# Optimization experiments

Measured on AMD Instinct MI355X. Metric: run time of the kernel, lower is better.

## Reference

```python
import jax, jax.numpy as jnp
import numpy as np

NUM_HEADS = 16
DIM = 1024
HEAD_DIM = DIM // NUM_HEADS
SCALE = HEAD_DIM ** -0.5


def setup_inputs() -> dict:
    key = jax.random.key(0)
    ks = jax.random.split(key, 6)
    b, n = 2, 1024
    x = jax.random.normal(ks[0], (b, n, DIM), dtype=jnp.float32)
    Wq = jax.random.normal(ks[1], (DIM, DIM), dtype=jnp.float32) * 0.02
    bq = jnp.zeros((DIM,), dtype=jnp.float32)
    Wkv = jax.random.normal(ks[2], (2 * DIM, DIM), dtype=jnp.float32) * 0.02
    bkv = jnp.zeros((2 * DIM,), dtype=jnp.float32)
    Wp = jax.random.normal(ks[3], (DIM, DIM), dtype=jnp.float32) * 0.02
    bp = jnp.zeros((DIM,), dtype=jnp.float32)
    return {"x": x, "Wq": Wq, "bq": bq, "Wkv": Wkv, "bkv": bkv, "Wp": Wp, "bp": bp}


def reference(x, Wq, bq, Wkv, bkv, Wp, bp):
    b, n, c = x.shape
    h, dh = NUM_HEADS, HEAD_DIM
    # self-attention: y = x
    q = (x @ Wq.T + bq).reshape(b, n, h, dh)              # bnhd
    kv = (x @ Wkv.T + bkv).reshape(b, n, 2, h, dh)
    k, v = kv[:, :, 0], kv[:, :, 1]                       # bmhd each
    attn = jnp.einsum('bnhd,bmhd->bnmh', q, k) * SCALE    # bnmh scores
    attn = jax.nn.softmax(attn, axis=2)                   # softmax over m
    out = jnp.einsum('bnmh,bmhd->bnhd', attn, v).reshape(b, n, c)
    out = out @ Wp.T + bp
    return (out, attn)
```

## Files before the change

kernel.cpp:

```cpp
#include <hip/hip_runtime.h>
#include <hip/hip_bf16.h>
#include <stdint.h>


#define NB   2
#define SEQ  1024
#define CDIM 1024
#define NH   16
#define HD   64
#define ROWS (NB*SEQ)
#define ATT_SCALE 0.125f

typedef __attribute__((ext_vector_type(8))) short bf16x8;
typedef __attribute__((ext_vector_type(4))) float f32x4;

#define MFMA16(a,b,c) __builtin_amdgcn_mfma_f32_16x16x32_bf16((a),(b),(c),0,0,0)

static __device__ __forceinline__ unsigned short f2bf(float f) {
  uint32_t x = __builtin_bit_cast(uint32_t, f);
  return (unsigned short)((x + 0x7fffu + ((x >> 16) & 1u)) >> 16);
}
static __device__ __forceinline__ float bf2f(unsigned short u) {
  uint32_t x = ((uint32_t)u) << 16;
  return __builtin_bit_cast(float, x);
}

static __device__ __forceinline__ void gl_lds16(const unsigned short* g,
                                                unsigned short* l) {
  __builtin_amdgcn_global_load_lds(
      (const __attribute__((address_space(1))) unsigned int*)g,
      (__attribute__((address_space(3))) unsigned int*)l,
      16, 0, 0);
}

__global__ __launch_bounds__(256) void k_convert(
    const float* __restrict__ x, const float* __restrict__ Wq,
    const float* __restrict__ Wkv, const float* __restrict__ Wp,
    unsigned short* __restrict__ Xhi, unsigned short* __restrict__ Xlo,
    unsigned short* __restrict__ Whi, unsigned short* __restrict__ Wlo)
{
  const int NX4 = ROWS*CDIM/4;
  const int NW4 = 4096*CDIM/4;
  int i = blockIdx.x*256 + threadIdx.x;
  float4 f;
  unsigned short* dh;
  unsigned short* dl;
  size_t o4;
  if (i < NX4) {
    f = ((const float4*)x)[i];
    dh = Xhi; dl = Xlo; o4 = (size_t)i*4;
  } else if (i < NX4 + NW4) {
    int w4 = i - NX4;
    int j = w4 >> 8;
    int c4 = w4 & 255;
    const float* ws = (j < 1024) ? Wq + (size_t)j*1024
                    : (j < 3072) ? Wkv + (size_t)(j-1024)*1024
                                 : Wp + (size_t)(j-3072)*1024;
    f = ((const float4*)ws)[c4];
    dh = Whi; dl = Wlo; o4 = (size_t)w4*4;
  } else return;
  float fv[4] = {f.x, f.y, f.z, f.w};
  unsigned int hp[2], lp[2];
  #pragma unroll
  for (int e = 0; e < 2; e++) {
    unsigned short h0 = f2bf(fv[e*2]),   l0 = f2bf(fv[e*2]   - bf2f(h0));
    unsigned short h1 = f2bf(fv[e*2+1]), l1 = f2bf(fv[e*2+1] - bf2f(h1));
    hp[e] = (unsigned)h0 | ((unsigned)h1 << 16);
    lp[e] = (unsigned)l0 | ((unsigned)l1 << 16);
  }
  *(uint2*)(dh + o4) = make_uint2(hp[0], hp[1]);
  *(uint2*)(dl + o4) = make_uint2(lp[0], lp[1]);
}

__global__ __launch_bounds__(256) void k_gemm_qkv(
    const unsigned short* __restrict__ Xhi, const unsigned short* __restrict__ Xlo,
    const unsigned short* __restrict__ Whi, const unsigned short* __restrict__ Wlo,
    const float* __restrict__ bq, const float* __restrict__ bkv,
    unsigned short* __restrict__ Qhi, unsigned short* __restrict__ Qlo,
    unsigned short* __restrict__ Khi, unsigned short* __restrict__ Klo,
    unsigned short* __restrict__ Vthi, unsigned short* __restrict__ Vtlo)
{
  __shared__ unsigned short smem[12288];
  unsigned short* sAh = smem;
  unsigned short* sAl = smem + 4096;
  unsigned short* sBh = smem + 8192;
  unsigned short* sBl = smem + 10240;
  const int tid = threadIdx.x, lane = tid & 63, wave = tid >> 6;
  const int wm = wave & 1, wn = wave >> 1;
  const int bn = blockIdx.x * 64, bm = blockIdx.y * 128;
  const int r = lane & 15, q = lane >> 4;
  const int crow = lane >> 2;
  const int cgsw = ((lane & 3) ^ ((crow >> 1) & 3)) * 8;
  const int qsw = (q ^ ((r >> 1) & 3)) * 8;

  f32x4 acc[4][2];
  #pragma unroll
  for (int i = 0; i < 4; i++)
    #pragma unroll
    for (int j = 0; j < 2; j++) {
      acc[i][j][0]=0.f; acc[i][j][1]=0.f; acc[i][j][2]=0.f; acc[i][j][3]=0.f;
    }

  for (int k0 = 0; k0 < CDIM; k0 += 32) {
    #pragma unroll
    for (int t = 0; t < 6; t++) {
      int c = wave + t*4;
      const unsigned short* gb; unsigned short* sb; int rr, grow;
      if (c < 8)        { gb=Xhi; sb=sAh; rr=c;    grow=bm; }
      else if (c < 16)  { gb=Xlo; sb=sAl; rr=c-8;  grow=bm; }
      else if (c < 20)  { gb=Whi; sb=sBh; rr=c-16; grow=bn; }
      else              { gb=Wlo; sb=sBl; rr=c-20; grow=bn; }
      int row = rr*16 + crow;
      gl_lds16(gb + (size_t)(grow + row)*CDIM + k0 + cgsw, sb + rr*512);
    }
    __syncthreads();
    bf16x8 ah[4], al[4], bh[2], bl[2];
    #pragma unroll
    for (int i = 0; i < 4; i++) {
      int oa = (wm*64 + i*16 + r)*32 + qsw;
      ah[i] = *(const bf16x8*)(sAh + oa);
      al[i] = *(const bf16x8*)(sAl + oa);
    }
    #pragma unroll
    for (int j = 0; j < 2; j++) {
      int ob = (wn*32 + j*16 + r)*32 + qsw;
      bh[j] = *(const bf16x8*)(sBh + ob);
      bl[j] = *(const bf16x8*)(sBl + ob);
    }
    #pragma unroll
    for (int i = 0; i < 4; i++)
      #pragma unroll
      for (int j = 0; j < 2; j++) {
        acc[i][j] = MFMA16(ah[i], bh[j], acc[i][j]);
        acc[i][j] = MFMA16(ah[i], bl[j], acc[i][j]);
        acc[i][j] = MFMA16(al[i], bh[j], acc[i][j]);
      }
    __syncthreads();
  }

  const int seg = bn >> 10;
  const float* bias = (seg == 0) ? (bq + bn) : (bkv + (bn - 1024));
  const float scl = (seg == 0) ? ATT_SCALE : 1.0f;
  float bj[2] = { bias[wn*32 + r], bias[wn*32 + 16 + r] };

  if (seg < 2) {
    unsigned short* dh = (seg == 0) ? Qhi : Khi;
    unsigned short* dl = (seg == 0) ? Qlo : Klo;
    const int ncol = bn & 1023;
    #pragma unroll
    for (int p = 0; p < 2; p++) {
      #pragma unroll
      for (int i = 0; i < 4; i++)
        #pragma unroll
        for (int j = 0; j < 2; j++)
          #pragma unroll
          for (int t = 0; t < 4; t++) {
            int m_l = wm*64 + i*16 + q*4 + t;
            int n_l = wn*32 + j*16 + r;
            float v2 = (acc[i][j][t] + bj[j]) * scl;
            unsigned short hv = f2bf(v2);
            unsigned short val = (p == 0) ? hv : f2bf(v2 - bf2f(hv));
            smem[m_l*72 + n_l] = val;
          }
      __syncthreads();
      unsigned short* dst = (p == 0) ? dh : dl;
      #pragma unroll
      for (int u = 0; u < 4; u++) {
        int s = u*256 + tid;
        int m_l = s >> 3, nseg = s & 7;
        uint4 vv = *(const uint4*)(smem + m_l*72 + nseg*8);
        *(uint4*)(dst + (size_t)(bm + m_l)*1024 + ncol + nseg*8) = vv;
      }
      __syncthreads();
    }
  } else {
    const int h = (bn - 2048) >> 6;
    const int b = bm >> 10, mm = bm & 1023;
    const size_t vtb = ((size_t)((b*NH + h)*HD))*SEQ + mm;
    #pragma unroll
    for (int p = 0; p < 2; p++) {
      #pragma unroll
      for (int i = 0; i < 4; i++)
        #pragma unroll
        for (int j = 0; j < 2; j++)
          #pragma unroll
          for (int t = 0; t < 4; t++) {
            int m_l = wm*64 + i*16 + q*4 + t;
            int d_l = wn*32 + j*16 + r;
            float v2 = acc[i][j][t] + bj[j];
            unsigned short hv = f2bf(v2);
            unsigned short val = (p == 0) ? hv : f2bf(v2 - bf2f(hv));
            smem[d_l*136 + m_l] = val;
          }
      __syncthreads();
      unsigned short* dst = (p == 0) ? Vthi : Vtlo;
      #pragma unroll
      for (int u = 0; u < 4; u++) {
        int s = u*256 + tid;
        int d_l = s >> 4, mseg = s & 15;
        uint4 vv = *(const uint4*)(smem + d_l*136 + mseg*8);
        *(uint4*)(dst + vtb + (size_t)d_l*SEQ + mseg*8) = vv;
      }
      __syncthreads();
    }
  }
}

struct EpiOut {
  const float* bp; float* out;
  __device__ __forceinline__ void operator()(int m, int n, float v) const {
    out[(size_t)m*1024 + n] = v + bp[n];
  }
};

template <int BM, int BN, int WM, int WN, class Epi>
__device__ __forceinline__ void gemm_core(
    const unsigned short* __restrict__ Ahi, const unsigned short* __restrict__ Alo, int lda,
    const unsigned short* __restrict__ Bhi, const unsigned short* __restrict__ Blo, int ldb,
    int K, const Epi& epi)
{
  constexpr int WAVES = WM*WN;
  constexpr int FM = BM/(WM*16), FN = BN/(WN*16);
  constexpr int CA = BM/16, CB = BN/16;
  constexpr int TOT = 2*(CA+CB);
  __shared__ unsigned short sAh[BM*32], sAl[BM*32], sBh[BN*32], sBl[BN*32];
  const int tid  = threadIdx.x;
  const int lane = tid & 63, wave = tid >> 6;
  const int wm = wave % WM, wn = wave / WM;
  const int bn = blockIdx.x * BN, bm = blockIdx.y * BM;
  const int r = lane & 15, q = lane >> 4;
  const int crow = lane >> 2;
  const int cgsw = ((lane & 3) ^ ((crow >> 1) & 3)) * 8;
  const int qsw = (q ^ ((r >> 1) & 3)) * 8;

  f32x4 acc[FM][FN];
  #pragma unroll
  for (int i = 0; i < FM; i++)
    #pragma unroll
    for (int j = 0; j < FN; j++) {
      acc[i][j][0]=0.f; acc[i][j][1]=0.f; acc[i][j][2]=0.f; acc[i][j][3]=0.f;
    }

  for (int k0 = 0; k0 < K; k0 += 32) {
    #pragma unroll
    for (int t = 0; t < TOT/WAVES; t++) {
      int c = wave + t*WAVES;
      const unsigned short* gb; unsigned short* sb; int rr, grow, ld;
      if (c < CA)            { gb=Ahi; sb=sAh; rr=c;         grow=bm; ld=lda; }
      else if (c < 2*CA)     { gb=Alo; sb=sAl; rr=c-CA;      grow=bm; ld=lda; }
      else if (c < 2*CA+CB)  { gb=Bhi; sb=sBh; rr=c-2*CA;    grow=bn; ld=ldb; }
      else                   { gb=Blo; sb=sBl; rr=c-2*CA-CB; grow=bn; ld=ldb; }
      int row = rr*16 + crow;
      gl_lds16(gb + (size_t)(grow + row)*ld + k0 + cgsw, sb + rr*512);
    }
    __syncthreads();
    bf16x8 ah[FM], al[FM], bh[FN], bl[FN];
    #pragma unroll
    for (int i = 0; i < FM; i++) {
      int oa = (wm*(BM/WM) + i*16 + r)*32 + qsw;
      ah[i] = *(const bf16x8*)(sAh + oa);
      al[i] = *(const bf16x8*)(sAl + oa);
    }
    #pragma unroll
    for (int j = 0; j < FN; j++) {
      int ob = (wn*(BN/WN) + j*16 + r)*32 + qsw;
      bh[j] = *(const bf16x8*)(sBh + ob);
      bl[j] = *(const bf16x8*)(sBl + ob);
    }
    #pragma unroll
    for (int i = 0; i < FM; i++)
      #pragma unroll
      for (int j = 0; j < FN; j++) {
        acc[i][j] = MFMA16(ah[i], bh[j], acc[i][j]);
        acc[i][j] = MFMA16(ah[i], bl[j], acc[i][j]);
        acc[i][j] = MFMA16(al[i], bh[j], acc[i][j]);
      }
    __syncthreads();
  }
  #pragma unroll
  for (int i = 0; i < FM; i++)
    #pragma unroll
    for (int j = 0; j < FN; j++)
      #pragma unroll
      for (int t = 0; t < 4; t++)
        epi(bm + wm*(BM/WM) + i*16 + q*4 + t, bn + wn*(BN/WN) + j*16 + r, acc[i][j][t]);
}

__global__ __launch_bounds__(512) void k_gemm_out(
    const unsigned short* OAhi, const unsigned short* OAlo,
    const unsigned short* Wphi, const unsigned short* Wplo,
    const float* bp, float* out)
{
  EpiOut e{bp, out};
  gemm_core<128,64,4,2>(OAhi, OAlo, CDIM, Wphi, Wplo, CDIM, CDIM, e);
}

__global__ __launch_bounds__(512, 4) void k_logits_softmax(
    const unsigned short* __restrict__ Qhi, const unsigned short* __restrict__ Qlo,
    const unsigned short* __restrict__ Khi, const unsigned short* __restrict__ Klo,
    unsigned short* __restrict__ P, float* __restrict__ F)
{
  int id = blockIdx.x + 32*(blockIdx.y + 16*blockIdx.z);
  id = (id & 7)*128 + (id >> 3);
  const int nt = id & 31, h = (id >> 5) & 15, b = id >> 9;
  const int n0 = nt*32;
  const int col0 = h*HD;
  __shared__ unsigned short sQ[2*32*64];
  __shared__ unsigned short sK[2][2*8192];
  __shared__ float redm[2][8][32];
  __shared__ float reds[8][32];
  __shared__ float musd[32][8];
  const int tid = threadIdx.x, lane = tid & 63, wave = tid >> 6;
  const int r = lane & 15, q = lane >> 4;
  const int drow = lane >> 3, dseg = (lane & 7) ^ drow;
  const int sw = r & 7;
  const size_t qrow0 = (size_t)b*SEQ + n0;
  const size_t krow0 = (size_t)b*SEQ;

  auto stageK = [&](int c, int buf) {
    unsigned short* dst = sK[buf];
    #pragma unroll
    for (int u = 0; u < 4; u++) {
      int cc = wave*4 + u;
      int p = cc >> 4, t = cc & 15;
      const unsigned short* g = p ? Klo : Khi;
      gl_lds16(g + (krow0 + (size_t)c*128 + t*8 + drow)*CDIM + col0 + dseg*8,
               dst + p*8192 + t*512);
    }
  };

  {
    int p = wave >> 2, t = wave & 3;
    const unsigned short* g = p ? Qlo : Qhi;
    gl_lds16(g + (qrow0 + t*8 + drow)*CDIM + col0 + dseg*8,
             sQ + p*2048 + t*512);
    stageK(0, 0);
  }
  __syncthreads();

  bf16x8 qh[2][2], ql[2][2];
  #pragma unroll
  for (int nf = 0; nf < 2; nf++)
    #pragma unroll
    for (int ks = 0; ks < 2; ks++) {
      int phys = (nf*16 + r)*64 + (((ks*4 + q) ^ sw))*8;
      qh[nf][ks] = *(const bf16x8*)(sQ + phys);
      ql[nf][ks] = *(const bf16x8*)(sQ + 2048 + phys);
    }

  const int mb = wave*16;
  float m_run[2] = {-1e30f, -1e30f}, s_run[2] = {0.f, 0.f};
  const size_t pbase = ((size_t)(b*NH + h)*SEQ + n0)*SEQ;

  for (int c = 0; c < 8; c++) {
    if (c < 7) stageK(c+1, (c+1)&1);
    const unsigned short* cur = sK[c&1];
    bf16x8 kh[2], kl[2];
    #pragma unroll
    for (int ks = 0; ks < 2; ks++) {
      int phys = (mb + r)*64 + (((ks*4 + q) ^ sw))*8;
      kh[ks] = *(const bf16x8*)(cur + phys);
      kl[ks] = *(const bf16x8*)(cur + 8192 + phys);
    }
    f32x4 acc[2];
    #pragma unroll
    for (int nf = 0; nf < 2; nf++) {
      acc[nf][0]=0.f; acc[nf][1]=0.f; acc[nf][2]=0.f; acc[nf][3]=0.f;
      #pragma unroll
      for (int ks = 0; ks < 2; ks++) {
        acc[nf] = MFMA16(kh[ks], qh[nf][ks], acc[nf]);
        acc[nf] = MFMA16(kl[ks], qh[nf][ks], acc[nf]);
        acc[nf] = MFMA16(kh[ks], ql[nf][ks], acc[nf]);
      }
    }
    float wmax[2];
    #pragma unroll
    for (int nf = 0; nf < 2; nf++) {
      float v = fmaxf(fmaxf(acc[nf][0], acc[nf][1]), fmaxf(acc[nf][2], acc[nf][3]));
      v = fmaxf(v, __shfl_xor(v, 16));
      v = fmaxf(v, __shfl_xor(v, 32));
      wmax[nf] = v;
    }
    if (q == 0) { redm[c&1][wave][r] = wmax[0]; redm[c&1][wave][16+r] = wmax[1]; }
    __syncthreads();
    #pragma unroll
    for (int nf = 0; nf < 2; nf++) {
      int row = nf*16 + r;
      float mc = redm[c&1][0][row];
      #pragma unroll
      for (int w2 = 1; w2 < 8; w2++) mc = fmaxf(mc, redm[c&1][w2][row]);
      float mnew = fmaxf(m_run[nf], mc);
      unsigned s0 = (unsigned)(__expf(acc[nf][0]-mnew)*65535.f + 0.5f);
      unsigned s1 = (unsigned)(__expf(acc[nf][1]-mnew)*65535.f + 0.5f);
      unsigned s2 = (unsigned)(__expf(acc[nf][2]-mnew)*65535.f + 0.5f);
      unsigned s3 = (unsigned)(__expf(acc[nf][3]-mnew)*65535.f + 0.5f);
      *(uint2*)(P + pbase + (size_t)row*SEQ + c*128 + mb + q*4) =
          make_uint2(s0 | (s1 << 16), s2 | (s3 << 16));
      s_run[nf] = s_run[nf]*__expf(m_run[nf]-mnew) + (float)(s0+s1+s2+s3);
      m_run[nf] = mnew;
      if (wave == 0 && q == 0) musd[row][c] = mnew;
    }
  }

  #pragma unroll
  for (int nf = 0; nf < 2; nf++) {
    float s = s_run[nf];
    s += __shfl_xor(s, 16);
    s += __shfl_xor(s, 32);
    if (q == 0) reds[wave][nf*16 + r] = s;
  }
  __syncthreads();
  if (tid < 32) {
    int row = tid;
    float S = 0.f;
    #pragma unroll
    for (int w2 = 0; w2 < 8; w2++) S += reds[w2][row];
    float mfin = musd[row][7];
    float inv = 1.0f / S;
    size_t fb = ((size_t)(b*NH + h)*SEQ + n0 + row)*8;
    #pragma unroll
    for (int c = 0; c < 8; c++)
      F[fb + c] = __expf(musd[row][c] - mfin) * inv;
  }
}

__global__ __launch_bounds__(256) void k_attn_write(
    const unsigned short* __restrict__ P, const float* __restrict__ F,
    float* __restrict__ attn)
{
  int T = blockIdx.x*256 + threadIdx.x;
  int b = T >> 20, rem = T & 1048575;
  int n = rem >> 10, m = rem & 1023;
  int c = m >> 7;
  const size_t pb = ((size_t)(b*NH)*SEQ + n)*SEQ + m;
  const size_t fb = ((size_t)(b*NH)*SEQ + n)*8 + c;
  float v[16];
  #pragma unroll
  for (int h = 0; h < 16; h++)
    v[h] = (float)P[pb + (size_t)h*SEQ*SEQ] * F[fb + (size_t)h*SEQ*8];
  size_t ob = ((size_t)(b*SEQ + n)*SEQ + m)*16;
  #pragma unroll
  for (int g = 0; g < 4; g++)
    *(float4*)(attn + ob + g*4) = make_float4(v[g*4], v[g*4+1], v[g*4+2], v[g*4+3]);
}

__global__ __launch_bounds__(256) void k_pv(
    const unsigned short* __restrict__ P, const float* __restrict__ F,
    const unsigned short* __restrict__ Vthi, const unsigned short* __restrict__ Vtlo,
    unsigned short* __restrict__ OAhi, unsigned short* __restrict__ OAlo)
{
  int id = blockIdx.x + 16*(blockIdx.y + 16*blockIdx.z);
  id = (id & 7)*64 + (id >> 3);
  int nt = id & 15, h = (id >> 4) & 15, b = id >> 8;
  int n0 = nt * 64;
  __shared__ unsigned short sPa[64*32], sPb[64*32], sVh[64*32], sVl[64*32];
  const int tid = threadIdx.x, lane = tid & 63, wave = tid >> 6;
  const int wm = wave & 1, wn = wave >> 1;
  const int r = lane & 15, q = lane >> 4;
  const int crow = lane >> 2;
  const int cgsw = ((lane & 3) ^ ((crow >> 1) & 3)) * 8;
  const int qsw = (q ^ ((r >> 1) & 3)) * 8;
  const size_t pbase = ((size_t)(b*NH + h))*SEQ*SEQ;
  const size_t vbase = ((size_t)(b*NH + h))*HD*SEQ;
  const size_t fbase = ((size_t)(b*NH + h))*SEQ*8;

  f32x4 acc[2][2], accF[2][2];
  #pragma unroll
  for (int i = 0; i < 2; i++)
    #pragma unroll
    for (int j = 0; j < 2; j++) {
      acc[i][j][0]=0.f; acc[i][j][1]=0.f; acc[i][j][2]=0.f; acc[i][j][3]=0.f;
      accF[i][j][0]=0.f; accF[i][j][1]=0.f; accF[i][j][2]=0.f; accF[i][j][3]=0.f;
    }

  for (int k0 = 0; k0 < SEQ; k0 += 32) {
    #pragma unroll
    for (int t = 0; t < 2; t++) {
      int c = wave + t*4;
      const unsigned short* gb = (c < 4) ? Vthi : Vtlo;
      unsigned short* sb = (c < 4) ? (unsigned short*)sVh : (unsigned short*)sVl;
      int rr = c & 3;
      int row = rr*16 + crow;
      gl_lds16(gb + vbase + (size_t)row*SEQ + k0 + cgsw, sb + rr*512);
    }
    {
      int row = tid >> 2, g = tid & 3, ch = g * 8;
      int gp = (g ^ ((row >> 1) & 3)) * 8;
      uint4 v = *(const uint4*)(P + pbase + (size_t)(n0 + row)*SEQ + k0 + ch);
      unsigned int wds[4] = {v.x, v.y, v.z, v.w};
      unsigned int pa[4], pb4[4];
      #pragma unroll
      for (int e = 0; e < 4; e++) {
        unsigned int lo16 = wds[e] & 0xFFFFu;
        unsigned int hi16 = wds[e] >> 16;
        unsigned int a0 = __builtin_bit_cast(uint32_t, (float)(lo16 & 0xFF00u)) >> 16;
        unsigned int b0 = __builtin_bit_cast(uint32_t, (float)(lo16 & 0x00FFu)) >> 16;
        unsigned int a1 = __builtin_bit_cast(uint32_t, (float)(hi16 & 0xFF00u)) >> 16;
        unsigned int b1 = __builtin_bit_cast(uint32_t, (float)(hi16 & 0x00FFu)) >> 16;
        pa[e]  = a0 | (a1 << 16);
        pb4[e] = b0 | (b1 << 16);
      }
      *(uint4*)(sPa + row*32 + gp) = make_uint4(pa[0],pa[1],pa[2],pa[3]);
      *(uint4*)(sPb + row*32 + gp) = make_uint4(pb4[0],pb4[1],pb4[2],pb4[3]);
    }
    __syncthreads();
    bf16x8 pa[2], pb2[2], vh[2], vl[2];
    #pragma unroll
    for (int i = 0; i < 2; i++) {
      int off = (wm*32 + i*16 + r)*32 + qsw;
      pa[i]  = *(const bf16x8*)(sPa + off);
      pb2[i] = *(const bf16x8*)(sPb + off);
    }
    #pragma unroll
    for (int j = 0; j < 2; j++) {
      int off = (wn*32 + j*16 + r)*32 + qsw;
      vh[j] = *(const bf16x8*)(sVh + off);
      vl[j] = *(const bf16x8*)(sVl + off);
    }
    #pragma unroll
    for (int i = 0; i < 2; i++)
      #pragma unroll
      for (int j = 0; j < 2; j++) {
        acc[i][j] = MFMA16(pa[i],  vh[j], acc[i][j]);
        acc[i][j] = MFMA16(pb2[i], vh[j], acc[i][j]);
        acc[i][j] = MFMA16(pa[i],  vl[j], acc[i][j]);
      }
    if ((k0 & 127) == 96) {
      int c = k0 >> 7;
      #pragma unroll
      for (int i = 0; i < 2; i++)
        #pragma unroll
        for (int t = 0; t < 4; t++) {
          int nn = n0 + wm*32 + i*16 + q*4 + t;
          float Fv = F[fbase + (size_t)nn*8 + c];
          #pragma unroll
          for (int j = 0; j < 2; j++) {
            accF[i][j][t] += acc[i][j][t] * Fv;
            acc[i][j][t] = 0.f;
          }
        }
    }
    __syncthreads();
  }
  #pragma unroll
  for (int i = 0; i < 2; i++)
    #pragma unroll
    for (int t = 0; t < 4; t++) {
      int nn = n0 + wm*32 + i*16 + q*4 + t;
      #pragma unroll
      for (int j = 0; j < 2; j++) {
        int d = wn*32 + j*16 + r;
        float val = accF[i][j][t];
        size_t o = (size_t)(b*SEQ + nn)*CDIM + h*HD + d;
        unsigned short hb = f2bf(val);
        OAhi[o] = hb; OAlo[o] = f2bf(val - bf2f(hb));
      }
    }
}

extern "C" void kernel_launch(void* const* d_in, const int* in_sizes, int n_in,
                              void* d_out, int out_size, void* d_ws, size_t ws_size,
                              hipStream_t stream)
{
  const float* x   = (const float*)d_in[0];
  const float* Wq  = (const float*)d_in[1];
  const float* bq  = (const float*)d_in[2];
  const float* Wkv = (const float*)d_in[3];
  const float* bkv = (const float*)d_in[4];
  const float* Wp  = (const float*)d_in[5];
  const float* bp  = (const float*)d_in[6];

  float* out  = (float*)d_out;
  float* attn = out + (size_t)ROWS*CDIM;

  char* w = (char*)d_ws;
  unsigned short* Xhi  = (unsigned short*)w; w += (size_t)ROWS*CDIM*2;
  unsigned short* Xlo  = (unsigned short*)w; w += (size_t)ROWS*CDIM*2;
  unsigned short* Whi  = (unsigned short*)w; w += (size_t)4096*CDIM*2;
  unsigned short* Wlo  = (unsigned short*)w; w += (size_t)4096*CDIM*2;
  unsigned short* Qhi  = (unsigned short*)w; w += (size_t)ROWS*CDIM*2;
  unsigned short* Qlo  = (unsigned short*)w; w += (size_t)ROWS*CDIM*2;
  unsigned short* Khi  = (unsigned short*)w; w += (size_t)ROWS*CDIM*2;
  unsigned short* Klo  = (unsigned short*)w; w += (size_t)ROWS*CDIM*2;
  unsigned short* Vthi = (unsigned short*)w; w += (size_t)NB*NH*HD*SEQ*2;
  unsigned short* Vtlo = (unsigned short*)w; w += (size_t)NB*NH*HD*SEQ*2;
  unsigned short* OAhi = (unsigned short*)w; w += (size_t)ROWS*CDIM*2;
  unsigned short* OAlo = (unsigned short*)w; w += (size_t)ROWS*CDIM*2;
  unsigned short* P    = (unsigned short*)w; w += (size_t)NB*NH*SEQ*SEQ*2;
  float*          Ftab = (float*)w;          w += (size_t)NB*NH*SEQ*8*4;

  k_convert<<<dim3((ROWS*CDIM/4 + 4096*CDIM/4)/256), 256, 0, stream>>>(
      x, Wq, Wkv, Wp, Xhi, Xlo, Whi, Wlo);

  k_gemm_qkv<<<dim3(3072/64, 2048/128), 256, 0, stream>>>(
      Xhi, Xlo, Whi, Wlo, bq, bkv, Qhi, Qlo, Khi, Klo, Vthi, Vtlo);

  k_logits_softmax<<<dim3(SEQ/32, NH, NB), 512, 0, stream>>>(
      Qhi, Qlo, Khi, Klo, P, Ftab);

  k_pv<<<dim3(SEQ/64, NH, NB), 256, 0, stream>>>(P, Ftab, Vthi, Vtlo, OAhi, OAlo);

  k_gemm_out<<<dim3(1024/64, 2048/128), 512, 0, stream>>>(
      OAhi, OAlo, Whi + (size_t)3072*CDIM, Wlo + (size_t)3072*CDIM, bp, out);

  k_attn_write<<<dim3((NB*SEQ*SEQ)/256), 256, 0, stream>>>(P, Ftab, attn);
}
```

Baseline: 350.2 us.

## Fuse logits/softmax and PV into one flash-style attention kernel

Merges the logits+softmax kernel with the separate P·V kernel into one kernel that keeps P tiles in shared memory and accumulates the output with online-softmax rescaling. The key chunk shrinks from 128 to 64, so the per-chunk factor table F grows to 16 entries per row. This removes the extra launch and the second pass that re-read the full quantized P matrix from global memory. In exchange each chunk now needs an extra barrier, more LDS, and more MFMA work per block.

Measured after the change: 345.6 us. Within noise of the previous version (-1.3%).

```diff
diff --git a/kernel.cpp b/kernel.cpp
--- a/kernel.cpp
+++ b/kernel.cpp
@@ -295,132 +295,194 @@
   gemm_core<128,64,4,2>(OAhi, OAlo, CDIM, Wphi, Wplo, CDIM, CDIM, e);
 }
 
-__global__ __launch_bounds__(512, 4) void k_logits_softmax(
+__global__ __launch_bounds__(512, 4) void k_attn_fused(
     const unsigned short* __restrict__ Qhi, const unsigned short* __restrict__ Qlo,
     const unsigned short* __restrict__ Khi, const unsigned short* __restrict__ Klo,
-    unsigned short* __restrict__ P, float* __restrict__ F)
+    const unsigned short* __restrict__ Vthi, const unsigned short* __restrict__ Vtlo,
+    unsigned short* __restrict__ P, float* __restrict__ F,
+    unsigned short* __restrict__ OAhi, unsigned short* __restrict__ OAlo)
 {
   int id = blockIdx.x + 32*(blockIdx.y + 16*blockIdx.z);
   id = (id & 7)*128 + (id >> 3);
   const int nt = id & 31, h = (id >> 5) & 15, b = id >> 9;
-  const int n0 = nt*32;
-  const int col0 = h*HD;
-  __shared__ unsigned short sQ[2*32*64];
-  __shared__ unsigned short sK[2][2*8192];
-  __shared__ float redm[2][8][32];
-  __shared__ float reds[8][32];
-  __shared__ float musd[32][8];
+  const int n0 = nt*32, col0 = h*HD;
+  __shared__ unsigned short sQ[2*2048];
+  __shared__ unsigned short sK[2][2*4096];
+  __shared__ unsigned short sV[2][2*4096];
+  __shared__ unsigned short sP[32*64];
+  __shared__ float redm[2][8][16];
+  float* musd  = (float*)sQ;
+  float* fac   = (float*)(sQ + 1024);
+  float* invSs = (float*)(sQ + 1088);
+  float* redsS = (float*)(sQ + 1152);
   const int tid = threadIdx.x, lane = tid & 63, wave = tid >> 6;
   const int r = lane & 15, q = lane >> 4;
   const int drow = lane >> 3, dseg = (lane & 7) ^ drow;
   const int sw = r & 7;
+  const int nf = wave >> 2;
+  const int mt = wave & 3;
   const size_t qrow0 = (size_t)b*SEQ + n0;
   const size_t krow0 = (size_t)b*SEQ;
+  const size_t vt0   = (size_t)(b*NH + h)*HD;
 
   auto stageK = [&](int c, int buf) {
-    unsigned short* dst = sK[buf];
-    #pragma unroll
-    for (int u = 0; u < 4; u++) {
-      int cc = wave*4 + u;
-      int p = cc >> 4, t = cc & 15;
+    #pragma unroll
+    for (int u = 0; u < 2; u++) {
+      int cc = wave*2 + u;
+      int p = cc >> 3, t = cc & 7;
       const unsigned short* g = p ? Klo : Khi;
-      gl_lds16(g + (krow0 + (size_t)c*128 + t*8 + drow)*CDIM + col0 + dseg*8,
-               dst + p*8192 + t*512);
+      gl_lds16(g + (krow0 + (size_t)c*64 + t*8 + drow)*CDIM + col0 + dseg*8,
+               sK[buf] + p*4096 + t*512);
+    }
+  };
+  auto stageV = [&](int c, int buf) {
+    #pragma unroll
+    for (int u = 0; u < 2; u++) {
+      int cc = wave*2 + u;
+      int p = cc >> 3, t = cc & 7;
+      const unsigned short* g = p ? Vtlo : Vthi;
+      gl_lds16(g + (vt0 + t*8 + drow)*SEQ + (size_t)c*64 + dseg*8,
+               sV[buf] + p*4096 + t*512);
     }
   };
 
   {
     int p = wave >> 2, t = wave & 3;
     const unsigned short* g = p ? Qlo : Qhi;
-    gl_lds16(g + (qrow0 + t*8 + drow)*CDIM + col0 + dseg*8,
-             sQ + p*2048 + t*512);
-    stageK(0, 0);
+    gl_lds16(g + (qrow0 + t*8 + drow)*CDIM + col0 + dseg*8, sQ + p*2048 + t*512);
+    stageK(0, 0); stageV(0, 0);
   }
   __syncthreads();
 
-  bf16x8 qh[2][2], ql[2][2];
-  #pragma unroll
-  for (int nf = 0; nf < 2; nf++)
+  bf16x8 qh[2], ql[2];
+  #pragma unroll
+  for (int ks = 0; ks < 2; ks++) {
+    int phys = (nf*16 + r)*64 + (((ks*4 + q) ^ sw))*8;
+    qh[ks] = *(const bf16x8*)(sQ + phys);
+    ql[ks] = *(const bf16x8*)(sQ + 2048 + phys);
+  }
+
+  float m_run = -1e30f, s_run = 0.f;
+  f32x4 accO; accO[0]=0.f; accO[1]=0.f; accO[2]=0.f; accO[3]=0.f;
+  const size_t pbase = ((size_t)(b*NH + h)*SEQ + n0)*SEQ;
+
+  for (int c = 0; c < 16; c++) {
+    const int buf = c & 1;
+    bf16x8 kh[2], kl[2];
     #pragma unroll
     for (int ks = 0; ks < 2; ks++) {
-      int phys = (nf*16 + r)*64 + (((ks*4 + q) ^ sw))*8;
-      qh[nf][ks] = *(const bf16x8*)(sQ + phys);
-      ql[nf][ks] = *(const bf16x8*)(sQ + 2048 + phys);
-    }
-
-  const int mb = wave*16;
-  float m_run[2] = {-1e30f, -1e30f}, s_run[2] = {0.f, 0.f};
-  const size_t pbase = ((size_t)(b*NH + h)*SEQ + n0)*SEQ;
-
-  for (int c = 0; c < 8; c++) {
-    if (c < 7) stageK(c+1, (c+1)&1);
-    const unsigned short* cur = sK[c&1];
-    bf16x8 kh[2], kl[2];
+      int phys = (mt*16 + r)*64 + (((ks*4 + q) ^ sw))*8;
+      kh[ks] = *(const bf16x8*)(sK[buf] + phys);
+      kl[ks] = *(const bf16x8*)(sK[buf] + 4096 + phys);
+    }
+    f32x4 acc; acc[0]=0.f; acc[1]=0.f; acc[2]=0.f; acc[3]=0.f;
     #pragma unroll
     for (int ks = 0; ks < 2; ks++) {
-      int phys = (mb + r)*64 + (((ks*4 + q) ^ sw))*8;
-      kh[ks] = *(const bf16x8*)(cur + phys);
-      kl[ks] = *(const bf16x8*)(cur + 8192 + phys);
-    }
-    f32x4 acc[2];
-    #pragma unroll
-    for (int nf = 0; nf < 2; nf++) {
-      acc[nf][0]=0.f; acc[nf][1]=0.f; acc[nf][2]=0.f; acc[nf][3]=0.f;
-      #pragma unroll
-      for (int ks = 0; ks < 2; ks++) {
-        acc[nf] = MFMA16(kh[ks], qh[nf][ks], acc[nf]);
-        acc[nf] = MFMA16(kl[ks], qh[nf][ks], acc[nf]);
-        acc[nf] = MFMA16(kh[ks], ql[nf][ks], acc[nf]);
-      }
-    }
-    float wmax[2];
-    #pragma unroll
-    for (int nf = 0; nf < 2; nf++) {
-      float v = fmaxf(fmaxf(acc[nf][0], acc[nf][1]), fmaxf(acc[nf][2], acc[nf][3]));
+      acc = MFMA16(kh[ks], qh[ks], acc);
+      acc = MFMA16(kl[ks], qh[ks], acc);
+      acc = MFMA16(kh[ks], ql[ks], acc);
+    }
+    {
+      float v = fmaxf(fmaxf(acc[0], acc[1]), fmaxf(acc[2], acc[3]));
       v = fmaxf(v, __shfl_xor(v, 16));
       v = fmaxf(v, __shfl_xor(v, 32));
-      wmax[nf] = v;
-    }
-    if (q == 0) { redm[c&1][wave][r] = wmax[0]; redm[c&1][wave][16+r] = wmax[1]; }
+      if (q == 0) redm[buf][wave][r] = v;
+    }
     __syncthreads();
-    #pragma unroll
-    for (int nf = 0; nf < 2; nf++) {
-      int row = nf*16 + r;
-      float mc = redm[c&1][0][row];
-      #pragma unroll
-      for (int w2 = 1; w2 < 8; w2++) mc = fmaxf(mc, redm[c&1][w2][row]);
-      float mnew = fmaxf(m_run[nf], mc);
-      unsigned s0 = (unsigned)(__expf(acc[nf][0]-mnew)*65535.f + 0.5f);
-      unsigned s1 = (unsigned)(__expf(acc[nf][1]-mnew)*65535.f + 0.5f);
-      unsigned s2 = (unsigned)(__expf(acc[nf][2]-mnew)*65535.f + 0.5f);
-      unsigned s3 = (unsigned)(__expf(acc[nf][3]-mnew)*65535.f + 0.5f);
-      *(uint2*)(P + pbase + (size_t)row*SEQ + c*128 + mb + q*4) =
-          make_uint2(s0 | (s1 << 16), s2 | (s3 << 16));
-      s_run[nf] = s_run[nf]*__expf(m_run[nf]-mnew) + (float)(s0+s1+s2+s3);
-      m_run[nf] = mnew;
-      if (wave == 0 && q == 0) musd[row][c] = mnew;
-    }
-  }
-
-  #pragma unroll
-  for (int nf = 0; nf < 2; nf++) {
-    float s = s_run[nf];
+    if (c < 15) { stageK(c+1, buf^1); stageV(c+1, buf^1); }
+    {
+      const int wg = nf*4;
+      float mc = redm[buf][wg][r];
+      #pragma unroll
+      for (int w2 = 1; w2 < 4; w2++) mc = fmaxf(mc, redm[buf][wg + w2][r]);
+      float mnew = fmaxf(m_run, mc);
+      if (wave == wg && q == 0) {
+        fac[nf*16 + r] = __expf(m_run - mnew);
+        musd[(nf*16 + r)*16 + c] = mnew;
+      }
+      unsigned s0 = (unsigned)(__expf(acc[0]-mnew)*65535.f + 0.5f);
+      unsigned s1 = (unsigned)(__expf(acc[1]-mnew)*65535.f + 0.5f);
+      unsigned s2 = (unsigned)(__expf(acc[2]-mnew)*65535.f + 0.5f);
+      unsigned s3 = (unsigned)(__expf(acc[3]-mnew)*65535.f + 0.5f);
+      uint2 pk = make_uint2(s0 | (s1 << 16), s2 | (s3 << 16));
+      const int row = nf*16 + r;
+      *(uint2*)(P + pbase + (size_t)row*SEQ + c*64 + mt*16 + q*4) = pk;
+      int gw = mt*2 + (q >> 1);
+      *(uint2*)(sP + row*64 + ((gw ^ (r & 7)) << 3) + (q & 1)*4) = pk;
+      s_run = s_run*__expf(m_run - mnew) + (float)(s0 + s1 + s2 + s3);
+      m_run = mnew;
+    }
+    __syncthreads();
+    {
+      float f0 = fac[nf*16 + q*4 + 0];
+      float f1 = fac[nf*16 + q*4 + 1];
+      float f2 = fac[nf*16 + q*4 + 2];
+      float f3 = fac[nf*16 + q*4 + 3];
+      accO[0] *= f0; accO[1] *= f1; accO[2] *= f2; accO[3] *= f3;
+      #pragma unroll
+      for (int kk = 0; kk < 2; kk++) {
+        int gr = kk*4 + q;
+        uint4 pv4 = *(const uint4*)(sP + (nf*16 + r)*64 + ((gr ^ (r & 7)) << 3));
+        unsigned int wds[4] = {pv4.x, pv4.y, pv4.z, pv4.w};
+        unsigned int pa_[4], pb_[4];
+        #pragma unroll
+        for (int e = 0; e < 4; e++) {
+          unsigned int lo16 = wds[e] & 0xFFFFu;
+          unsigned int hi16 = wds[e] >> 16;
+          unsigned int a0 = __builtin_bit_cast(uint32_t, (float)(lo16 & 0xFF00u)) >> 16;
+          unsigned int b0 = __builtin_bit_cast(uint32_t, (float)(lo16 & 0x00FFu)) >> 16;
+          unsigned int a1 = __builtin_bit_cast(uint32_t, (float)(hi16 & 0xFF00u)) >> 16;
+          unsigned int b1 = __builtin_bit_cast(uint32_t, (float)(hi16 & 0x00FFu)) >> 16;
+          pa_[e] = a0 | (a1 << 16);
+          pb_[e] = b0 | (b1 << 16);
+        }
+        bf16x8 pa = __builtin_bit_cast(bf16x8, make_uint4(pa_[0],pa_[1],pa_[2],pa_[3]));
+        bf16x8 pb = __builtin_bit_cast(bf16x8, make_uint4(pb_[0],pb_[1],pb_[2],pb_[3]));
+        int physv = (mt*16 + r)*64 + (((kk*4 + q) ^ sw))*8;
+        bf16x8 vh = *(const bf16x8*)(sV[buf] + physv);
+        bf16x8 vl = *(const bf16x8*)(sV[buf] + 4096 + physv);
+        accO = MFMA16(pa, vh, accO);
+        accO = MFMA16(pb, vh, accO);
+        accO = MFMA16(pa, vl, accO);
+      }
+    }
+  }
+
+  {
+    float s = s_run;
     s += __shfl_xor(s, 16);
     s += __shfl_xor(s, 32);
-    if (q == 0) reds[wave][nf*16 + r] = s;
+    if (q == 0) redsS[wave*16 + r] = s;
   }
   __syncthreads();
   if (tid < 32) {
     int row = tid;
-    float S = 0.f;
-    #pragma unroll
-    for (int w2 = 0; w2 < 8; w2++) S += reds[w2][row];
-    float mfin = musd[row][7];
+    int wg = (row >> 4)*4, rr = row & 15;
+    float S = redsS[wg*16 + rr] + redsS[(wg+1)*16 + rr]
+            + redsS[(wg+2)*16 + rr] + redsS[(wg+3)*16 + rr];
+    float mfin = musd[row*16 + 15];
     float inv = 1.0f / S;
-    size_t fb = ((size_t)(b*NH + h)*SEQ + n0 + row)*8;
-    #pragma unroll
-    for (int c = 0; c < 8; c++)
-      F[fb + c] = __expf(musd[row][c] - mfin) * inv;
+    invSs[row] = inv;
+    size_t fb = ((size_t)(b*NH + h)*SEQ + n0 + row)*16;
+    #pragma unroll
+    for (int c = 0; c < 16; c++)
+      F[fb + c] = __expf(musd[row*16 + c] - mfin) * inv;
+  }
+  __syncthreads();
+  {
+    float i0 = invSs[nf*16 + q*4 + 0];
+    float i1 = invSs[nf*16 + q*4 + 1];
+    float i2 = invSs[nf*16 + q*4 + 2];
+    float i3 = invSs[nf*16 + q*4 + 3];
+    float vals[4] = {accO[0]*i0, accO[1]*i1, accO[2]*i2, accO[3]*i3};
+    #pragma unroll
+    for (int t = 0; t < 4; t++) {
+      int nn = n0 + nf*16 + q*4 + t;
+      int d = mt*16 + r;
+      size_t o = (size_t)(b*SEQ + nn)*CDIM + h*HD + d;
+      unsigned short hb = f2bf(vals[t]);
+      OAhi[o] = hb; OAlo[o] = f2bf(vals[t] - bf2f(hb));
+    }
   }
 }
 
@@ -431,131 +493,17 @@
   int T = blockIdx.x*256 + threadIdx.x;
   int b = T >> 20, rem = T & 1048575;
   int n = rem >> 10, m = rem & 1023;
-  int c = m >> 7;
+  int c = m >> 6;
   const size_t pb = ((size_t)(b*NH)*SEQ + n)*SEQ + m;
-  const size_t fb = ((size_t)(b*NH)*SEQ + n)*8 + c;
+  const size_t fb = ((size_t)(b*NH)*SEQ + n)*16 + c;
   float v[16];
   #pragma unroll
   for (int h = 0; h < 16; h++)
-    v[h] = (float)P[pb + (size_t)h*SEQ*SEQ] * F[fb + (size_t)h*SEQ*8];
+    v[h] = (float)P[pb + (size_t)h*SEQ*SEQ] * F[fb + (size_t)h*SEQ*16];
   size_t ob = ((size_t)(b*SEQ + n)*SEQ + m)*16;
   #pragma unroll
   for (int g = 0; g < 4; g++)
     *(float4*)(attn + ob + g*4) = make_float4(v[g*4], v[g*4+1], v[g*4+2], v[g*4+3]);
-}
-
-__global__ __launch_bounds__(256) void k_pv(
-    const unsigned short* __restrict__ P, const float* __restrict__ F,
-    const unsigned short* __restrict__ Vthi, const unsigned short* __restrict__ Vtlo,
-    unsigned short* __restrict__ OAhi, unsigned short* __restrict__ OAlo)
-{
-  int id = blockIdx.x + 16*(blockIdx.y + 16*blockIdx.z);
-  id = (id & 7)*64 + (id >> 3);
-  int nt = id & 15, h = (id >> 4) & 15, b = id >> 8;
-  int n0 = nt * 64;
-  __shared__ unsigned short sPa[64*32], sPb[64*32], sVh[64*32], sVl[64*32];
-  const int tid = threadIdx.x, lane = tid & 63, wave = tid >> 6;
-  const int wm = wave & 1, wn = wave >> 1;
-  const int r = lane & 15, q = lane >> 4;
-  const int crow = lane >> 2;
-  const int cgsw = ((lane & 3) ^ ((crow >> 1) & 3)) * 8;
-  const int qsw = (q ^ ((r >> 1) & 3)) * 8;
-  const size_t pbase = ((size_t)(b*NH + h))*SEQ*SEQ;
-  const size_t vbase = ((size_t)(b*NH + h))*HD*SEQ;
-  const size_t fbase = ((size_t)(b*NH + h))*SEQ*8;
-
-  f32x4 acc[2][2], accF[2][2];
-  #pragma unroll
-  for (int i = 0; i < 2; i++)
-    #pragma unroll
-    for (int j = 0; j < 2; j++) {
-      acc[i][j][0]=0.f; acc[i][j][1]=0.f; acc[i][j][2]=0.f; acc[i][j][3]=0.f;
-      accF[i][j][0]=0.f; accF[i][j][1]=0.f; accF[i][j][2]=0.f; accF[i][j][3]=0.f;
-    }
-
-  for (int k0 = 0; k0 < SEQ; k0 += 32) {
-    #pragma unroll
-    for (int t = 0; t < 2; t++) {
-      int c = wave + t*4;
-      const unsigned short* gb = (c < 4) ? Vthi : Vtlo;
-      unsigned short* sb = (c < 4) ? (unsigned short*)sVh : (unsigned short*)sVl;
-      int rr = c & 3;
-      int row = rr*16 + crow;
-      gl_lds16(gb + vbase + (size_t)row*SEQ + k0 + cgsw, sb + rr*512);
-    }
-    {
-      int row = tid >> 2, g = tid & 3, ch = g * 8;
-      int gp = (g ^ ((row >> 1) & 3)) * 8;
-      uint4 v = *(const uint4*)(P + pbase + (size_t)(n0 + row)*SEQ + k0 + ch);
-      unsigned int wds[4] = {v.x, v.y, v.z, v.w};
-      unsigned int pa[4], pb4[4];
-      #pragma unroll
-      for (int e = 0; e < 4; e++) {
-        unsigned int lo16 = wds[e] & 0xFFFFu;
-        unsigned int hi16 = wds[e] >> 16;
-        unsigned int a0 = __builtin_bit_cast(uint32_t, (float)(lo16 & 0xFF00u)) >> 16;
-        unsigned int b0 = __builtin_bit_cast(uint32_t, (float)(lo16 & 0x00FFu)) >> 16;
-        unsigned int a1 = __builtin_bit_cast(uint32_t, (float)(hi16 & 0xFF00u)) >> 16;
-        unsigned int b1 = __builtin_bit_cast(uint32_t, (float)(hi16 & 0x00FFu)) >> 16;
-        pa[e]  = a0 | (a1 << 16);
-        pb4[e] = b0 | (b1 << 16);
-      }
-      *(uint4*)(sPa + row*32 + gp) = make_uint4(pa[0],pa[1],pa[2],pa[3]);
-      *(uint4*)(sPb + row*32 + gp) = make_uint4(pb4[0],pb4[1],pb4[2],pb4[3]);
-    }
-    __syncthreads();
-    bf16x8 pa[2], pb2[2], vh[2], vl[2];
-    #pragma unroll
-    for (int i = 0; i < 2; i++) {
-      int off = (wm*32 + i*16 + r)*32 + qsw;
-      pa[i]  = *(const bf16x8*)(sPa + off);
-      pb2[i] = *(const bf16x8*)(sPb + off);
-    }
-    #pragma unroll
-    for (int j = 0; j < 2; j++) {
-      int off = (wn*32 + j*16 + r)*32 + qsw;
-      vh[j] = *(const bf16x8*)(sVh + off);
-      vl[j] = *(const bf16x8*)(sVl + off);
-    }
-    #pragma unroll
-    for (int i = 0; i < 2; i++)
-      #pragma unroll
-      for (int j = 0; j < 2; j++) {
-        acc[i][j] = MFMA16(pa[i],  vh[j], acc[i][j]);
-        acc[i][j] = MFMA16(pb2[i], vh[j], acc[i][j]);
-        acc[i][j] = MFMA16(pa[i],  vl[j], acc[i][j]);
-      }
-    if ((k0 & 127) == 96) {
-      int c = k0 >> 7;
-      #pragma unroll
-      for (int i = 0; i < 2; i++)
-        #pragma unroll
-        for (int t = 0; t < 4; t++) {
-          int nn = n0 + wm*32 + i*16 + q*4 + t;
-          float Fv = F[fbase + (size_t)nn*8 + c];
-          #pragma unroll
-          for (int j = 0; j < 2; j++) {
-            accF[i][j][t] += acc[i][j][t] * Fv;
-            acc[i][j][t] = 0.f;
-          }
-        }
-    }
-    __syncthreads();
-  }
-  #pragma unroll
-  for (int i = 0; i < 2; i++)
-    #pragma unroll
-    for (int t = 0; t < 4; t++) {
-      int nn = n0 + wm*32 + i*16 + q*4 + t;
-      #pragma unroll
-      for (int j = 0; j < 2; j++) {
-        int d = wn*32 + j*16 + r;
-        float val = accF[i][j][t];
-        size_t o = (size_t)(b*SEQ + nn)*CDIM + h*HD + d;
-        unsigned short hb = f2bf(val);
-        OAhi[o] = hb; OAlo[o] = f2bf(val - bf2f(hb));
-      }
-    }
 }
 
 extern "C" void kernel_launch(void* const* d_in, const int* in_sizes, int n_in,
@@ -587,7 +535,7 @@
   unsigned short* OAhi = (unsigned short*)w; w += (size_t)ROWS*CDIM*2;
   unsigned short* OAlo = (unsigned short*)w; w += (size_t)ROWS*CDIM*2;
   unsigned short* P    = (unsigned short*)w; w += (size_t)NB*NH*SEQ*SEQ*2;
-  float*          Ftab = (float*)w;          w += (size_t)NB*NH*SEQ*8*4;
+  float*          Ftab = (float*)w;          w += (size_t)NB*NH*SEQ*16*4;
 
   k_convert<<<dim3((ROWS*CDIM/4 + 4096*CDIM/4)/256), 256, 0, stream>>>(
       x, Wq, Wkv, Wp, Xhi, Xlo, Whi, Wlo);
@@ -595,10 +543,8 @@
   k_gemm_qkv<<<dim3(3072/64, 2048/128), 256, 0, stream>>>(
       Xhi, Xlo, Whi, Wlo, bq, bkv, Qhi, Qlo, Khi, Klo, Vthi, Vtlo);
 
-  k_logits_softmax<<<dim3(SEQ/32, NH, NB), 512, 0, stream>>>(
-      Qhi, Qlo, Khi, Klo, P, Ftab);
-
-  k_pv<<<dim3(SEQ/64, NH, NB), 256, 0, stream>>>(P, Ftab, Vthi, Vtlo, OAhi, OAlo);
+  k_attn_fused<<<dim3(SEQ/32, NH, NB), 512, 0, stream>>>(
+      Qhi, Qlo, Khi, Klo, Vthi, Vtlo, P, Ftab, OAhi, OAlo);
 
   k_gemm_out<<<dim3(1024/64, 2048/128), 512, 0, stream>>>(
       OAhi, OAlo, Whi + (size_t)3072*CDIM, Wlo + (size_t)3072*CDIM, bp, out);
```
